# Kernel optimization log

Measured on AMD Instinct MI355X. Metric: run time of the kernel, lower is better.

Reference implementation:

```python
import jax, jax.numpy as jnp
import numpy as np

B, IN_DIM, HID, ODE_STEPS = 8192, 1024, 1024, 6
DT = 1.0


def setup_inputs() -> dict:
    key = jax.random.key(0)
    ks = jax.random.split(key, 8)
    s = 0.02  # init scale for stability
    return {
        "x": jax.random.normal(ks[0], (B, IN_DIM), dtype=jnp.float32),
        "h": jax.random.normal(ks[1], (B, HID), dtype=jnp.float32),
        "log_tau": jnp.zeros((HID,), dtype=jnp.float32),
        "W_in_w": jax.random.normal(ks[2], (HID, IN_DIM), dtype=jnp.float32) * s,
        "W_in_b": jnp.zeros((HID,), dtype=jnp.float32),
        "W_rec_w": jax.random.normal(ks[3], (HID, HID), dtype=jnp.float32) * s,
        "W_gate_w": jax.random.normal(ks[4], (HID, IN_DIM + HID), dtype=jnp.float32) * s,
        "W_gate_b": jnp.zeros((HID,), dtype=jnp.float32),
    }


def reference(x, h, log_tau, W_in_w, W_in_b, W_rec_w, W_gate_w, W_gate_b):
    # torch Linear: y = x @ W.T + b, W:(out,in)
    tau = jnp.exp(log_tau)                      # (HID,)
    input_drive = x @ W_in_w.T + W_in_b         # (B,HID), loop-invariant
    # W_gate acts on concat([x, h]); split into x-block and h-block.
    Wg_x = W_gate_w[:, :IN_DIM]
    Wg_h = W_gate_w[:, IN_DIM:]
    gate_x = x @ Wg_x.T + W_gate_b              # (B,HID), loop-invariant
    sub_dt = DT / ODE_STEPS
    scale = sub_dt / tau                        # (HID,)

    def step(h, _):
        gate = jax.nn.sigmoid(gate_x + h @ Wg_h.T)
        f = -h + gate * jnp.tanh(input_drive + h @ W_rec_w.T)
        return h + scale * f, None

    h, _ = jax.lax.scan(step, h, None, length=ODE_STEPS)
    return (h, h)
```

## Files before the change

kernel.cpp:

```cpp
#include <hip/hip_runtime.h>
#include <hip/hip_bf16.h>
#include <stdint.h>

#define B_DIM 8192
#define IN_DIMC 1024
#define HIDC 1024
#define K_DIM 1024
#define ODE_STEPS 6

typedef float f32x4 __attribute__((ext_vector_type(4)));
typedef short bf16x8 __attribute__((ext_vector_type(8)));
typedef unsigned short u16x8 __attribute__((ext_vector_type(8)));

__device__ __forceinline__ float bf2f(unsigned short u) {
    union { unsigned int u; float f; } c; c.u = ((unsigned int)u) << 16; return c.f;
}
__device__ __forceinline__ unsigned short f2bf(float f) {
    union { float f; unsigned int u; } c; c.f = f;
    unsigned int u = c.u;
    return (unsigned short)((u + 0x7fffu + ((u >> 16) & 1u)) >> 16);
}
__device__ __forceinline__ float fast_tanh(float x) {
    float e = __expf(2.0f * x);
    return 1.0f - 2.0f / (e + 1.0f);
}

constexpr size_t XN    = (size_t)B_DIM * IN_DIMC;
constexpr size_t HN    = (size_t)B_DIM * HIDC;
constexpr size_t WINN  = (size_t)HIDC * IN_DIMC;
constexpr size_t WRECN = (size_t)HIDC * HIDC;
constexpr size_t WGN   = (size_t)HIDC * (IN_DIMC + HIDC);
constexpr size_t TOTQ  = (XN + HN + WINN + WRECN + WGN) / 4;

__global__ __launch_bounds__(256) void convert_all(
    const float* __restrict__ x, const float* __restrict__ h,
    const float* __restrict__ win, const float* __restrict__ wrec,
    const float* __restrict__ wgate,
    unsigned short* __restrict__ x_bf, unsigned short* __restrict__ h_bf,
    unsigned short* __restrict__ win_bf, unsigned short* __restrict__ wrec_bf,
    unsigned short* __restrict__ wgx_bf, unsigned short* __restrict__ wgh_bf)
{
    size_t q = (size_t)blockIdx.x * 256 + threadIdx.x;
    if (q >= TOTQ) return;
    size_t e = q * 4;
    const float* src; unsigned short* dst; size_t si, di;
    if (e < XN)                          { src = x;    si = e;                       dst = x_bf;    di = si; }
    else if (e < XN + HN)                { src = h;    si = e - XN;                  dst = h_bf;    di = si; }
    else if (e < XN + HN + WINN)         { src = win;  si = e - XN - HN;             dst = win_bf;  di = si; }
    else if (e < XN + HN + WINN + WRECN) { src = wrec; si = e - XN - HN - WINN;      dst = wrec_bf; di = si; }
    else {
        size_t i = e - XN - HN - WINN - WRECN;
        size_t row = i >> 11, col = i & 2047;
        src = wgate; si = i;
        if (col < 1024) { dst = wgx_bf; di = row * 1024 + col; }
        else            { dst = wgh_bf; di = row * 1024 + (col - 1024); }
    }
    float4 v = *(const float4*)(src + si);
    ushort4 o;
    o.x = f2bf(v.x); o.y = f2bf(v.y); o.z = f2bf(v.z); o.w = f2bf(v.w);
    *(ushort4*)(dst + di) = o;
}

constexpr int BM = 256, BN = 128, BK = 32;
constexpr int NT = HIDC / BN;
constexpr int GRID = (B_DIM / BM) * NT;
constexpr int NKT = K_DIM / BK;

__device__ __forceinline__ void gload_lds16(const void* g, void* l) {
    __builtin_amdgcn_global_load_lds(
        (const __attribute__((address_space(1))) void*)g,
        (__attribute__((address_space(3))) void*)l, 16, 0, 0);
}

#define MFMA_BF16 __builtin_amdgcn_mfma_f32_16x16x32_bf16

#define DS_READ(D, A_, O) \
    asm volatile("ds_read_b128 %0, %1 offset:" O : "=v"(D) : "v"(A_))

#define STAGE4(SQ, KE) do {                                                   \
    gload_lds16(sA  + (KE),          &SMEM[(SQ) * 8192 + dA]);                \
    gload_lds16(sA  + 16384 + (KE),  &SMEM[(SQ) * 8192 + dA + 512]);          \
    gload_lds16(sB1 + (KE),          &SMEM[32768 + (SQ) * 4096 + dB]);        \
    gload_lds16(sB2 + (KE),          &SMEM[49152 + (SQ) * 4096 + dB]);        \
} while (0)

#define KITER(P, VM, DO_STG, SQ, KE)                                          \
    {                                                                         \
        if (DO_STG) STAGE4(SQ, KE);                                           \
        asm volatile("s_waitcnt vmcnt(" VM ")" ::: "memory");                 \
        __builtin_amdgcn_sched_barrier(0);                                    \
        asm volatile("s_barrier" ::: "memory");                               \
        bf16x8 a0, a1, a2, a3, x0, x1, x2, x3, y0, y1, y2, y3;                \
        const unsigned aA  = rdA  + (P) * 16384;                              \
        const unsigned aB1 = rdB1 + (P) * 8192;                               \
        const unsigned aB2 = rdB2 + (P) * 8192;                               \
        DS_READ(a0, aA, "0");    DS_READ(a1, aA, "1024");                     \
        DS_READ(a2, aA, "2048"); DS_READ(a3, aA, "3072");                     \
        DS_READ(x0, aB1, "0");    DS_READ(x1, aB1, "1024");                   \
        DS_READ(x2, aB1, "2048"); DS_READ(x3, aB1, "3072");                   \
        DS_READ(y0, aB2, "0");    DS_READ(y1, aB2, "1024");                   \
        DS_READ(y2, aB2, "2048"); DS_READ(y3, aB2, "3072");                   \
        asm volatile("s_waitcnt lgkmcnt(4)" ::: "memory");                    \
        __builtin_amdgcn_sched_barrier(0);                                    \
        __builtin_amdgcn_s_setprio(1);                                        \
        acc1[0][0] = MFMA_BF16(a0, x0, acc1[0][0], 0, 0, 0);                  \
        acc1[1][0] = MFMA_BF16(a1, x0, acc1[1][0], 0, 0, 0);                  \
        acc1[2][0] = MFMA_BF16(a2, x0, acc1[2][0], 0, 0, 0);                  \
        acc1[3][0] = MFMA_BF16(a3, x0, acc1[3][0], 0, 0, 0);                  \
        acc1[0][1] = MFMA_BF16(a0, x1, acc1[0][1], 0, 0, 0);                  \
        acc1[1][1] = MFMA_BF16(a1, x1, acc1[1][1], 0, 0, 0);                  \
        acc1[2][1] = MFMA_BF16(a2, x1, acc1[2][1], 0, 0, 0);                  \
        acc1[3][1] = MFMA_BF16(a3, x1, acc1[3][1], 0, 0, 0);                  \
        acc1[0][2] = MFMA_BF16(a0, x2, acc1[0][2], 0, 0, 0);                  \
        acc1[1][2] = MFMA_BF16(a1, x2, acc1[1][2], 0, 0, 0);                  \
        acc1[2][2] = MFMA_BF16(a2, x2, acc1[2][2], 0, 0, 0);                  \
        acc1[3][2] = MFMA_BF16(a3, x2, acc1[3][2], 0, 0, 0);                  \
        acc1[0][3] = MFMA_BF16(a0, x3, acc1[0][3], 0, 0, 0);                  \
        acc1[1][3] = MFMA_BF16(a1, x3, acc1[1][3], 0, 0, 0);                  \
        acc1[2][3] = MFMA_BF16(a2, x3, acc1[2][3], 0, 0, 0);                  \
        acc1[3][3] = MFMA_BF16(a3, x3, acc1[3][3], 0, 0, 0);                  \
        __builtin_amdgcn_s_setprio(0);                                        \
        asm volatile("s_waitcnt lgkmcnt(0)" ::: "memory");                    \
        __builtin_amdgcn_sched_barrier(0);                                    \
        __builtin_amdgcn_s_setprio(1);                                        \
        acc2[0][0] = MFMA_BF16(a0, y0, acc2[0][0], 0, 0, 0);                  \
        acc2[1][0] = MFMA_BF16(a1, y0, acc2[1][0], 0, 0, 0);                  \
        acc2[2][0] = MFMA_BF16(a2, y0, acc2[2][0], 0, 0, 0);                  \
        acc2[3][0] = MFMA_BF16(a3, y0, acc2[3][0], 0, 0, 0);                  \
        acc2[0][1] = MFMA_BF16(a0, y1, acc2[0][1], 0, 0, 0);                  \
        acc2[1][1] = MFMA_BF16(a1, y1, acc2[1][1], 0, 0, 0);                  \
        acc2[2][1] = MFMA_BF16(a2, y1, acc2[2][1], 0, 0, 0);                  \
        acc2[3][1] = MFMA_BF16(a3, y1, acc2[3][1], 0, 0, 0);                  \
        acc2[0][2] = MFMA_BF16(a0, y2, acc2[0][2], 0, 0, 0);                  \
        acc2[1][2] = MFMA_BF16(a1, y2, acc2[1][2], 0, 0, 0);                  \
        acc2[2][2] = MFMA_BF16(a2, y2, acc2[2][2], 0, 0, 0);                  \
        acc2[3][2] = MFMA_BF16(a3, y2, acc2[3][2], 0, 0, 0);                  \
        acc2[0][3] = MFMA_BF16(a0, y3, acc2[0][3], 0, 0, 0);                  \
        acc2[1][3] = MFMA_BF16(a1, y3, acc2[1][3], 0, 0, 0);                  \
        acc2[2][3] = MFMA_BF16(a2, y3, acc2[2][3], 0, 0, 0);                  \
        acc2[3][3] = MFMA_BF16(a3, y3, acc2[3][3], 0, 0, 0);                  \
        __builtin_amdgcn_s_setprio(0);                                        \
        asm volatile("s_barrier" ::: "memory");                               \
    }

template<bool STEP>
__global__ __launch_bounds__(512, 2) void ltc_gemm(
    const unsigned short* __restrict__ A,
    const unsigned short* __restrict__ B1,
    const unsigned short* __restrict__ B2,
    const unsigned short* __restrict__ GXID,
    const float* __restrict__ h_init,
    float* __restrict__ h_nat,
    const float* __restrict__ log_tau,
    float* __restrict__ h_out,
    float* __restrict__ h_out2,
    unsigned short* __restrict__ hbf_out,
    const float* __restrict__ bias1, const float* __restrict__ bias2,
    unsigned short* __restrict__ GXID_out)
{
    __shared__ __attribute__((aligned(16))) unsigned short SMEM[65536];

    const int tid = threadIdx.x;
    const int w = tid >> 6, l = tid & 63;
    const int bid = (blockIdx.x & 7) * (GRID / 8) + (blockIdx.x >> 3);
    const int mt = bid / NT, nt = bid % NT;
    const int m0 = mt * BM, n0 = nt * BN;
    const int wm = (w >> 1) * 64, wn = (w & 1) * 64;
    const int lm = l & 15, lq = l >> 4;

    const int lrg = l >> 2;
    const int gsl = (l & 3) ^ ((lrg >> 1) & 3);
    const unsigned short* sA  = A  + (size_t)(m0 + w * 32 + lrg) * K_DIM + gsl * 8;
    const unsigned short* sB1 = B1 + (size_t)(n0 + w * 16 + lrg) * K_DIM + gsl * 8;
    const unsigned short* sB2 = B2 + (size_t)(n0 + w * 16 + lrg) * K_DIM + gsl * 8;
    const int dA = w * 1024;
    const int dB = w * 512;

    const int phys = lq ^ ((lm >> 1) & 3);
    const unsigned smem0 = (unsigned)(uintptr_t)&SMEM[0];
    const unsigned rdA  = smem0 +          (wm + lm) * 64 + phys * 16;
    const unsigned rdB1 = smem0 + 65536 + (wn + lm) * 64 + phys * 16;
    const unsigned rdB2 = smem0 + 98304 + (wn + lm) * 64 + phys * 16;

    f32x4 acc1[4][4], acc2[4][4];
    f32x4 z4 = {0.f, 0.f, 0.f, 0.f};
    #pragma unroll
    for (int i = 0; i < 4; i++)
        #pragma unroll
        for (int j = 0; j < 4; j++) { acc1[i][j] = z4; acc2[i][j] = z4; }

    STAGE4(0, 0); STAGE4(1, 32); STAGE4(2, 64);

    #pragma unroll 1
    for (int tb = 0; tb < NKT - 4; tb += 4) {
        const int ke = (tb + 3) * BK;
        KITER(0, "12", true, 3, ke);
        KITER(1, "12", true, 0, ke + 32);
        KITER(2, "12", true, 1, ke + 64);
        KITER(3, "12", true, 2, ke + 96);
    }
    KITER(0, "12", true, 3, (NKT - 1) * BK);
    KITER(1, "8",  false, 0, 0);
    KITER(2, "4",  false, 0, 0);
    KITER(3, "0",  false, 0, 0);

    constexpr float subdt = 1.0f / (float)ODE_STEPS;
    const size_t wslot = (((size_t)bid * 8 + w) * 16) * 64 + l;

    float pc1[4], pc2[4];
    #pragma unroll
    for (int ni = 0; ni < 4; ni++) {
        const int gn = n0 + wn + ni * 16 + lm;
        if (STEP) {
            pc1[ni] = subdt * __expf(-log_tau[gn]);
        } else {
            pc1[ni] = bias1[gn];
            pc2[ni] = bias2[gn];
        }
    }

    #pragma unroll
    for (int mi = 0; mi < 4; mi++) {
        #pragma unroll
        for (int ni = 0; ni < 4; ni++) {
            const int gmb = m0 + wm + mi * 16 + lq * 4;
            const int gn  = n0 + wn + ni * 16 + lm;
            const size_t slot = wslot + (size_t)(mi * 4 + ni) * 64;
            if (STEP) {
                const float sc = pc1[ni];
                u16x8 gi = *(const u16x8*)&GXID[slot * 8];
                f32x4 st;
                if (h_init) {
                    #pragma unroll
                    for (int r = 0; r < 4; r++)
                        st[r] = h_init[(size_t)(gmb + r) * HIDC + gn];
                } else {
                    st = *(const f32x4*)&h_nat[slot * 4];
                }
                f32x4 hn;
                #pragma unroll
                for (int r = 0; r < 4; r++) {
                    float gx = bf2f((unsigned short)gi[r])     + acc1[mi][ni][r];
                    float dr = bf2f((unsigned short)gi[4 + r]) + acc2[mi][ni][r];
                    float gt = fast_tanh(dr) / (1.0f + __expf(-gx));
                    hn[r] = fmaf(sc, gt - st[r], st[r]);
                }
                if (h_out) {
                    #pragma unroll
                    for (int r = 0; r < 4; r++) {
                        size_t idx = (size_t)(gmb + r) * HIDC + gn;
                        h_out[idx]  = hn[r];
                        h_out2[idx] = hn[r];
                    }
                } else {
                    *(f32x4*)&h_nat[slot * 4] = hn;
                    #pragma unroll
                    for (int r = 0; r < 4; r++)
                        hbf_out[(size_t)(gmb + r) * HIDC + gn] = f2bf(hn[r]);
                }
            } else {
                u16x8 o;
                #pragma unroll
                for (int r = 0; r < 4; r++) {
                    o[r]     = f2bf(acc1[mi][ni][r] + pc1[ni]);
                    o[4 + r] = f2bf(acc2[mi][ni][r] + pc2[ni]);
                }
                *(u16x8*)&GXID_out[slot * 8] = o;
            }
        }
    }
}

extern "C" void kernel_launch(void* const* d_in, const int* in_sizes, int n_in,
                              void* d_out, int out_size, void* d_ws, size_t ws_size,
                              hipStream_t stream)
{
    const float* x    = (const float*)d_in[0];
    const float* h    = (const float*)d_in[1];
    const float* ltau = (const float*)d_in[2];
    const float* winw = (const float*)d_in[3];
    const float* winb = (const float*)d_in[4];
    const float* wrec = (const float*)d_in[5];
    const float* wg   = (const float*)d_in[6];
    const float* wgb  = (const float*)d_in[7];

    char* ws = (char*)d_ws;
    unsigned short* x_bf    = (unsigned short*)ws; ws += XN * 2;
    unsigned short* h_bf0   = (unsigned short*)ws; ws += HN * 2;
    unsigned short* h_bf1   = (unsigned short*)ws; ws += HN * 2;
    unsigned short* win_bf  = (unsigned short*)ws; ws += WINN * 2;
    unsigned short* wrec_bf = (unsigned short*)ws; ws += WRECN * 2;
    unsigned short* wgx_bf  = (unsigned short*)ws; ws += WINN * 2;
    unsigned short* wgh_bf  = (unsigned short*)ws; ws += WRECN * 2;
    unsigned short* GXID    = (unsigned short*)ws; ws += HN * 2 * 2;
    float*          h_nat   = (float*)ws;          ws += HN * 4;

    float* hout  = (float*)d_out;
    float* hout2 = hout + (size_t)B_DIM * HIDC;

    convert_all<<<(int)(TOTQ / 256), 256, 0, stream>>>(
        x, h, winw, wrec, wg, x_bf, h_bf0, win_bf, wrec_bf, wgx_bf, wgh_bf);

    ltc_gemm<false><<<GRID, 512, 0, stream>>>(
        x_bf, wgx_bf, win_bf,
        nullptr, nullptr, nullptr, nullptr, nullptr, nullptr, nullptr,
        wgb, winb, GXID);

    unsigned short* hbf[2] = {h_bf0, h_bf1};
    for (int s = 0; s < ODE_STEPS; s++) {
        const bool last = (s == ODE_STEPS - 1);
        ltc_gemm<true><<<GRID, 512, 0, stream>>>(
            hbf[s & 1], wgh_bf, wrec_bf,
            GXID,
            (s == 0) ? h : nullptr,
            h_nat, ltau,
            last ? hout : nullptr, last ? hout2 : nullptr,
            last ? nullptr : hbf[(s + 1) & 1],
            nullptr, nullptr, nullptr);
    }
}
```

Measured before the change: 459.2 us.

## Software-pipeline LDS fragment reads one k-tile ahead with single barrier per iteration

```diff
diff --git a/kernel.cpp b/kernel.cpp
--- a/kernel.cpp
+++ b/kernel.cpp
@@ -84,64 +84,74 @@
     gload_lds16(sB2 + (KE),          &SMEM[49152 + (SQ) * 4096 + dB]);        \
 } while (0)
 
-#define KITER(P, VM, DO_STG, SQ, KE)                                          \
-    {                                                                         \
-        if (DO_STG) STAGE4(SQ, KE);                                           \
-        asm volatile("s_waitcnt vmcnt(" VM ")" ::: "memory");                 \
-        __builtin_amdgcn_sched_barrier(0);                                    \
-        asm volatile("s_barrier" ::: "memory");                               \
-        bf16x8 a0, a1, a2, a3, x0, x1, x2, x3, y0, y1, y2, y3;                \
-        const unsigned aA  = rdA  + (P) * 16384;                              \
-        const unsigned aB1 = rdB1 + (P) * 8192;                               \
-        const unsigned aB2 = rdB2 + (P) * 8192;                               \
-        DS_READ(a0, aA, "0");    DS_READ(a1, aA, "1024");                     \
-        DS_READ(a2, aA, "2048"); DS_READ(a3, aA, "3072");                     \
-        DS_READ(x0, aB1, "0");    DS_READ(x1, aB1, "1024");                   \
-        DS_READ(x2, aB1, "2048"); DS_READ(x3, aB1, "3072");                   \
-        DS_READ(y0, aB2, "0");    DS_READ(y1, aB2, "1024");                   \
-        DS_READ(y2, aB2, "2048"); DS_READ(y3, aB2, "3072");                   \
-        asm volatile("s_waitcnt lgkmcnt(4)" ::: "memory");                    \
-        __builtin_amdgcn_sched_barrier(0);                                    \
-        __builtin_amdgcn_s_setprio(1);                                        \
-        acc1[0][0] = MFMA_BF16(a0, x0, acc1[0][0], 0, 0, 0);                  \
-        acc1[1][0] = MFMA_BF16(a1, x0, acc1[1][0], 0, 0, 0);                  \
-        acc1[2][0] = MFMA_BF16(a2, x0, acc1[2][0], 0, 0, 0);                  \
-        acc1[3][0] = MFMA_BF16(a3, x0, acc1[3][0], 0, 0, 0);                  \
-        acc1[0][1] = MFMA_BF16(a0, x1, acc1[0][1], 0, 0, 0);                  \
-        acc1[1][1] = MFMA_BF16(a1, x1, acc1[1][1], 0, 0, 0);                  \
-        acc1[2][1] = MFMA_BF16(a2, x1, acc1[2][1], 0, 0, 0);                  \
-        acc1[3][1] = MFMA_BF16(a3, x1, acc1[3][1], 0, 0, 0);                  \
-        acc1[0][2] = MFMA_BF16(a0, x2, acc1[0][2], 0, 0, 0);                  \
-        acc1[1][2] = MFMA_BF16(a1, x2, acc1[1][2], 0, 0, 0);                  \
-        acc1[2][2] = MFMA_BF16(a2, x2, acc1[2][2], 0, 0, 0);                  \
-        acc1[3][2] = MFMA_BF16(a3, x2, acc1[3][2], 0, 0, 0);                  \
-        acc1[0][3] = MFMA_BF16(a0, x3, acc1[0][3], 0, 0, 0);                  \
-        acc1[1][3] = MFMA_BF16(a1, x3, acc1[1][3], 0, 0, 0);                  \
-        acc1[2][3] = MFMA_BF16(a2, x3, acc1[2][3], 0, 0, 0);                  \
-        acc1[3][3] = MFMA_BF16(a3, x3, acc1[3][3], 0, 0, 0);                  \
-        __builtin_amdgcn_s_setprio(0);                                        \
-        asm volatile("s_waitcnt lgkmcnt(0)" ::: "memory");                    \
-        __builtin_amdgcn_sched_barrier(0);                                    \
-        __builtin_amdgcn_s_setprio(1);                                        \
-        acc2[0][0] = MFMA_BF16(a0, y0, acc2[0][0], 0, 0, 0);                  \
-        acc2[1][0] = MFMA_BF16(a1, y0, acc2[1][0], 0, 0, 0);                  \
-        acc2[2][0] = MFMA_BF16(a2, y0, acc2[2][0], 0, 0, 0);                  \
-        acc2[3][0] = MFMA_BF16(a3, y0, acc2[3][0], 0, 0, 0);                  \
-        acc2[0][1] = MFMA_BF16(a0, y1, acc2[0][1], 0, 0, 0);                  \
-        acc2[1][1] = MFMA_BF16(a1, y1, acc2[1][1], 0, 0, 0);                  \
-        acc2[2][1] = MFMA_BF16(a2, y1, acc2[2][1], 0, 0, 0);                  \
-        acc2[3][1] = MFMA_BF16(a3, y1, acc2[3][1], 0, 0, 0);                  \
-        acc2[0][2] = MFMA_BF16(a0, y2, acc2[0][2], 0, 0, 0);                  \
-        acc2[1][2] = MFMA_BF16(a1, y2, acc2[1][2], 0, 0, 0);                  \
-        acc2[2][2] = MFMA_BF16(a2, y2, acc2[2][2], 0, 0, 0);                  \
-        acc2[3][2] = MFMA_BF16(a3, y2, acc2[3][2], 0, 0, 0);                  \
-        acc2[0][3] = MFMA_BF16(a0, y3, acc2[0][3], 0, 0, 0);                  \
-        acc2[1][3] = MFMA_BF16(a1, y3, acc2[1][3], 0, 0, 0);                  \
-        acc2[2][3] = MFMA_BF16(a2, y3, acc2[2][3], 0, 0, 0);                  \
-        acc2[3][3] = MFMA_BF16(a3, y3, acc2[3][3], 0, 0, 0);                  \
-        __builtin_amdgcn_s_setprio(0);                                        \
-        asm volatile("s_barrier" ::: "memory");                               \
-    }
+#define RD_AFX(FA, FX, a0,a1,a2,a3, b0,b1,b2,b3) do {                         \
+    DS_READ(FA##_0, rdA,  a0); DS_READ(FA##_1, rdA,  a1);                     \
+    DS_READ(FA##_2, rdA,  a2); DS_READ(FA##_3, rdA,  a3);                     \
+    DS_READ(FX##_0, rdB1, b0); DS_READ(FX##_1, rdB1, b1);                     \
+    DS_READ(FX##_2, rdB1, b2); DS_READ(FX##_3, rdB1, b3);                     \
+} while (0)
+#define RD_YQ(y0,y1,y2,y3) do {                                               \
+    DS_READ(fy_0, rdB2, y0); DS_READ(fy_1, rdB2, y1);                         \
+    DS_READ(fy_2, rdB2, y2); DS_READ(fy_3, rdB2, y3);                         \
+} while (0)
+
+#define RD_AFX_B0(FA, FX) RD_AFX(FA, FX, "0","1024","2048","3072",            "0","1024","2048","3072")
+#define RD_AFX_B1(FA, FX) RD_AFX(FA, FX, "16384","17408","18432","19456",     "8192","9216","10240","11264")
+#define RD_AFX_B2(FA, FX) RD_AFX(FA, FX, "32768","33792","34816","35840",     "16384","17408","18432","19456")
+#define RD_AFX_B3(FA, FX) RD_AFX(FA, FX, "49152","50176","51200","52224",     "24576","25600","26624","27648")
+#define RD_Y_B0() RD_YQ("0","1024","2048","3072")
+#define RD_Y_B1() RD_YQ("8192","9216","10240","11264")
+#define RD_Y_B2() RD_YQ("16384","17408","18432","19456")
+#define RD_Y_B3() RD_YQ("24576","25600","26624","27648")
+
+#define MFMA16(ACC, F0, F1, F2, F3, G0, G1, G2, G3) do {                      \
+    ACC[0][0] = MFMA_BF16(F0, G0, ACC[0][0], 0, 0, 0);                        \
+    ACC[1][0] = MFMA_BF16(F1, G0, ACC[1][0], 0, 0, 0);                        \
+    ACC[2][0] = MFMA_BF16(F2, G0, ACC[2][0], 0, 0, 0);                        \
+    ACC[3][0] = MFMA_BF16(F3, G0, ACC[3][0], 0, 0, 0);                        \
+    ACC[0][1] = MFMA_BF16(F0, G1, ACC[0][1], 0, 0, 0);                        \
+    ACC[1][1] = MFMA_BF16(F1, G1, ACC[1][1], 0, 0, 0);                        \
+    ACC[2][1] = MFMA_BF16(F2, G1, ACC[2][1], 0, 0, 0);                        \
+    ACC[3][1] = MFMA_BF16(F3, G1, ACC[3][1], 0, 0, 0);                        \
+    ACC[0][2] = MFMA_BF16(F0, G2, ACC[0][2], 0, 0, 0);                        \
+    ACC[1][2] = MFMA_BF16(F1, G2, ACC[1][2], 0, 0, 0);                        \
+    ACC[2][2] = MFMA_BF16(F2, G2, ACC[2][2], 0, 0, 0);                        \
+    ACC[3][2] = MFMA_BF16(F3, G2, ACC[3][2], 0, 0, 0);                        \
+    ACC[0][3] = MFMA_BF16(F0, G3, ACC[0][3], 0, 0, 0);                        \
+    ACC[1][3] = MFMA_BF16(F1, G3, ACC[1][3], 0, 0, 0);                        \
+    ACC[2][3] = MFMA_BF16(F2, G3, ACC[2][3], 0, 0, 0);                        \
+    ACC[3][3] = MFMA_BF16(F3, G3, ACC[3][3], 0, 0, 0);                        \
+} while (0)
+
+#define WAIT_SB(S) do { asm volatile("s_waitcnt " S ::: "memory");            \
+                        __builtin_amdgcn_sched_barrier(0); } while (0)
+
+#define KITER6(PS, KE, VM, RDY, RDN, Fc, Xc, Fr, Xr) do {                     \
+    STAGE4(PS, KE);                                                           \
+    WAIT_SB("vmcnt(" VM ")");                                                 \
+    asm volatile("s_barrier" ::: "memory");                                   \
+    RDY();                                                                    \
+    RDN(Fr, Xr);                                                              \
+    WAIT_SB("lgkmcnt(12)");                                                   \
+    __builtin_amdgcn_s_setprio(1);                                            \
+    MFMA16(acc1, Fc##_0, Fc##_1, Fc##_2, Fc##_3, Xc##_0, Xc##_1, Xc##_2, Xc##_3); \
+    WAIT_SB("lgkmcnt(8)");                                                    \
+    MFMA16(acc2, Fc##_0, Fc##_1, Fc##_2, Fc##_3, fy_0, fy_1, fy_2, fy_3);     \
+    __builtin_amdgcn_s_setprio(0);                                            \
+} while (0)
+
+#define KITER6_NS(VM, RDY, RDN, Fc, Xc, Fr, Xr) do {                          \
+    WAIT_SB("vmcnt(" VM ")");                                                 \
+    asm volatile("s_barrier" ::: "memory");                                   \
+    RDY();                                                                    \
+    RDN(Fr, Xr);                                                              \
+    WAIT_SB("lgkmcnt(12)");                                                   \
+    __builtin_amdgcn_s_setprio(1);                                            \
+    MFMA16(acc1, Fc##_0, Fc##_1, Fc##_2, Fc##_3, Xc##_0, Xc##_1, Xc##_2, Xc##_3); \
+    WAIT_SB("lgkmcnt(8)");                                                    \
+    MFMA16(acc2, Fc##_0, Fc##_1, Fc##_2, Fc##_3, fy_0, fy_1, fy_2, fy_3);     \
+    __builtin_amdgcn_s_setprio(0);                                            \
+} while (0)
 
 template<bool STEP>
 __global__ __launch_bounds__(512, 2) void ltc_gemm(
@@ -189,20 +199,32 @@
         #pragma unroll
         for (int j = 0; j < 4; j++) { acc1[i][j] = z4; acc2[i][j] = z4; }
 
+    bf16x8 fa0_0, fa0_1, fa0_2, fa0_3, fx0_0, fx0_1, fx0_2, fx0_3;
+    bf16x8 fa1_0, fa1_1, fa1_2, fa1_3, fx1_0, fx1_1, fx1_2, fx1_3;
+    bf16x8 fy_0, fy_1, fy_2, fy_3;
+
     STAGE4(0, 0); STAGE4(1, 32); STAGE4(2, 64);
+    WAIT_SB("vmcnt(8)");
+    asm volatile("s_barrier" ::: "memory");
+    RD_AFX_B0(fa0, fx0);
 
     #pragma unroll 1
-    for (int tb = 0; tb < NKT - 4; tb += 4) {
-        const int ke = (tb + 3) * BK;
-        KITER(0, "12", true, 3, ke);
-        KITER(1, "12", true, 0, ke + 32);
-        KITER(2, "12", true, 1, ke + 64);
-        KITER(3, "12", true, 2, ke + 96);
-    }
-    KITER(0, "12", true, 3, (NKT - 1) * BK);
-    KITER(1, "8",  false, 0, 0);
-    KITER(2, "4",  false, 0, 0);
-    KITER(3, "0",  false, 0, 0);
+    for (int tb = 0; tb < 28; tb += 4) {
+        KITER6(3, (tb + 3) * 32, "8", RD_Y_B0, RD_AFX_B1, fa0, fx0, fa1, fx1);
+        KITER6(0, (tb + 4) * 32, "8", RD_Y_B1, RD_AFX_B2, fa1, fx1, fa0, fx0);
+        KITER6(1, (tb + 5) * 32, "8", RD_Y_B2, RD_AFX_B3, fa0, fx0, fa1, fx1);
+        KITER6(2, (tb + 6) * 32, "8", RD_Y_B3, RD_AFX_B0, fa1, fx1, fa0, fx0);
+    }
+    KITER6(3, 31 * 32, "8", RD_Y_B0, RD_AFX_B1, fa0, fx0, fa1, fx1);
+    KITER6_NS("4", RD_Y_B1, RD_AFX_B2, fa1, fx1, fa0, fx0);
+    KITER6_NS("0", RD_Y_B2, RD_AFX_B3, fa0, fx0, fa1, fx1);
+    RD_Y_B3();
+    WAIT_SB("lgkmcnt(4)");
+    __builtin_amdgcn_s_setprio(1);
+    MFMA16(acc1, fa1_0, fa1_1, fa1_2, fa1_3, fx1_0, fx1_1, fx1_2, fx1_3);
+    WAIT_SB("lgkmcnt(0)");
+    MFMA16(acc2, fa1_0, fa1_1, fa1_2, fa1_3, fy_0, fy_1, fy_2, fy_3);
+    __builtin_amdgcn_s_setprio(0);
 
     constexpr float subdt = 1.0f / (float)ODE_STEPS;
     const size_t wslot = (((size_t)bid * 8 + w) * 16) * 64 + l;
```

Measured after the change: 486.3 us. +5.9%, slower.
